# Optimization experiments

Measured on AMD Instinct MI355X. Metric: run time of the kernel, lower is better.

Reference implementation:

```python
import jax, jax.numpy as jnp
import numpy as np

IN_CHANNELS = 1024
NUM_HEADS = 16
HEAD_DIM = IN_CHANNELS // NUM_HEADS  # 64
N = 65536


def setup_inputs() -> dict:
    key = jax.random.key(0)
    k_x, k_wq, k_bq, k_wo, k_bo = jax.random.split(key, 5)
    x = jax.random.normal(k_x, (N, IN_CHANNELS), dtype=jnp.float32)
    # torch Linear convention: weight is [out_features, in_features]
    w_qkv = jax.random.normal(k_wq, (3 * IN_CHANNELS, IN_CHANNELS), dtype=jnp.float32) * 0.02
    b_qkv = jax.random.normal(k_bq, (3 * IN_CHANNELS,), dtype=jnp.float32) * 0.02
    w_out = jax.random.normal(k_wo, (IN_CHANNELS, IN_CHANNELS), dtype=jnp.float32) * 0.02
    b_out = jax.random.normal(k_bo, (IN_CHANNELS,), dtype=jnp.float32) * 0.02
    return {"x": x, "w_qkv": w_qkv, "b_qkv": b_qkv, "w_out": w_out, "b_out": b_out}


def reference(x, w_qkv, b_qkv, w_out, b_out):
    n = x.shape[0]
    scale = HEAD_DIM ** (-0.5)
    qkv = x @ w_qkv.T + b_qkv                       # [N, 3C]
    qkv = qkv.reshape(n, NUM_HEADS, 3 * HEAD_DIM)    # [N, H, 3D]
    q, k, v = jnp.split(qkv, 3, axis=-1)             # each [N, H, D]
    # attention over the HEAD dimension: [N, H, H] tiny score matrices
    attn = jnp.einsum('nhd,ngd->nhg', q * scale, k)
    attn = jax.nn.softmax(attn, axis=-1)
    out = jnp.einsum('nhg,ngd->nhd', attn, v)        # [N, H, D]
    out = out.reshape(n, NUM_HEADS * HEAD_DIM)       # [N, C]
    return out @ w_out.T + b_out
```

## Files before the change

### kernel.cpp

```cpp
#include <hip/hip_runtime.h>
#include <hip/hip_bf16.h>

#define N_TOK 65536
#define C_DIM 1024

typedef __hip_bfloat16 bf16;
typedef short short8 __attribute__((ext_vector_type(8)));
typedef short short4v __attribute__((ext_vector_type(4)));
typedef float f32x4 __attribute__((ext_vector_type(4)));

__device__ __forceinline__ void gload_lds16(const void* g, void* l) {
  __builtin_amdgcn_global_load_lds(
      (const __attribute__((address_space(1))) void*)g,
      (__attribute__((address_space(3))) void*)l, 16, 0, 0);
}

__global__ void cvt_kernel(const float* __restrict__ in, bf16* __restrict__ out, long n4) {
  long i = (long)blockIdx.x * blockDim.x + threadIdx.x;
  const long stride = (long)gridDim.x * blockDim.x;
  for (; i < n4; i += stride) {
    const float4 v = ((const float4*)in)[i];
    union { bf16 h[4]; uint2 u; } p;
    p.h[0] = __float2bfloat16(v.x);
    p.h[1] = __float2bfloat16(v.y);
    p.h[2] = __float2bfloat16(v.z);
    p.h[3] = __float2bfloat16(v.w);
    ((uint2*)out)[i] = p.u;
  }
}

template<bool OUT_BF16>
__global__ __launch_bounds__(256, 2) void gemm_bt(
    const bf16* __restrict__ A, const bf16* __restrict__ B,
    const float* __restrict__ bias, void* __restrict__ Cv,
    int M, int N, int K, int ntiles) {
  __shared__ __attribute__((aligned(16))) bf16 As[2][128 * 32];
  __shared__ __attribute__((aligned(16))) bf16 Bs[2][128 * 32];
  const int t = threadIdx.x;
  const int bid = blockIdx.x;
  const int mt = bid / ntiles, ntl = bid % ntiles;
  const long m0 = (long)mt * 128, n0 = (long)ntl * 128;
  const bf16* Ab = A + m0 * K;
  const bf16* Bb = B + n0 * K;

  const int lane = t & 63, wid = t >> 6;
  const int wr = (wid >> 1) * 64, wc = (wid & 1) * 64;
  const int lr = lane & 15, lk = (lane >> 4) * 8;

  f32x4 acc[4][4];
#pragma unroll
  for (int i = 0; i < 4; i++)
#pragma unroll
    for (int j = 0; j < 4; j++) acc[i][j] = f32x4{0.f, 0.f, 0.f, 0.f};

  auto stage = [&](int buf, int kt) {
    const long kbase = (long)kt * 32;
#pragma unroll
    for (int r = 0; r < 2; ++r) {
      const int lin = r * 256 + t;
      const int mrow = lin >> 2, ke = (lin & 3) * 8;
      gload_lds16(Ab + (long)mrow * K + kbase + ke, &As[buf][lin * 8]);
      gload_lds16(Bb + (long)mrow * K + kbase + ke, &Bs[buf][lin * 8]);
    }
  };

  stage(0, 0);
  const int KT = K / 32;
  int cur = 0;
  for (int kt = 0; kt < KT; ++kt) {
    __syncthreads();
    if (kt + 1 < KT) stage(cur ^ 1, kt + 1);
    short8 a[4], b[4];
#pragma unroll
    for (int i = 0; i < 4; i++)
      a[i] = *(const short8*)&As[cur][(wr + i * 16 + lr) * 32 + lk];
#pragma unroll
    for (int j = 0; j < 4; j++)
      b[j] = *(const short8*)&Bs[cur][(wc + j * 16 + lr) * 32 + lk];
#pragma unroll
    for (int i = 0; i < 4; i++)
#pragma unroll
      for (int j = 0; j < 4; j++)
        acc[i][j] = __builtin_amdgcn_mfma_f32_16x16x32_bf16(a[i], b[j], acc[i][j], 0, 0, 0);
    cur ^= 1;
  }

  float bv[4];
#pragma unroll
  for (int j = 0; j < 4; j++) bv[j] = bias[n0 + wc + j * 16 + lr];
#pragma unroll
  for (int i = 0; i < 4; i++) {
    const long rbase = m0 + wr + i * 16 + ((lane >> 4) << 2);
#pragma unroll
    for (int q = 0; q < 4; q++) {
      const long row = rbase + q;
#pragma unroll
      for (int j = 0; j < 4; j++) {
        const float v = acc[i][j][q] + bv[j];
        const long col = n0 + wc + j * 16 + lr;
        if constexpr (OUT_BF16)
          ((bf16*)Cv)[row * N + col] = __float2bfloat16(v);
        else
          ((float*)Cv)[row * N + col] = v;
      }
    }
  }
}

__global__ __launch_bounds__(256) void attn_kernel(const bf16* __restrict__ qkv,
                                                   bf16* __restrict__ out) {
  const int t = threadIdx.x, w = t >> 6, lane = t & 63;
  const long tok = (long)blockIdx.x * 4 + w;
  const bf16* base = qkv + tok * 3072;
  const int r = lane & 15, g4 = lane >> 4;

  const short8 ka0 = *(const short8*)(base + r * 192 + 64 + g4 * 8);
  const short8 ka1 = *(const short8*)(base + r * 192 + 96 + g4 * 8);
  const short8 qb0 = *(const short8*)(base + r * 192 + g4 * 8);
  const short8 qb1 = *(const short8*)(base + r * 192 + 32 + g4 * 8);
  f32x4 c = {0.f, 0.f, 0.f, 0.f};
  c = __builtin_amdgcn_mfma_f32_16x16x32_bf16(ka0, qb0, c, 0, 0, 0);
  c = __builtin_amdgcn_mfma_f32_16x16x32_bf16(ka1, qb1, c, 0, 0, 0);

  float s0 = c[0] * 0.125f, s1 = c[1] * 0.125f, s2 = c[2] * 0.125f, s3 = c[3] * 0.125f;
  float mx = fmaxf(fmaxf(s0, s1), fmaxf(s2, s3));
  mx = fmaxf(mx, __shfl_xor(mx, 16, 64));
  mx = fmaxf(mx, __shfl_xor(mx, 32, 64));
  const float e0 = __expf(s0 - mx), e1 = __expf(s1 - mx);
  const float e2 = __expf(s2 - mx), e3 = __expf(s3 - mx);
  float sum = e0 + e1 + e2 + e3;
  sum += __shfl_xor(sum, 16, 64);
  sum += __shfl_xor(sum, 32, 64);
  const float inv = 1.0f / sum;

#if __has_builtin(__builtin_amdgcn_mfma_f32_16x16x16bf16_1k)
  union { bf16 h[4]; short4v v; } pa;
  pa.h[0] = __float2bfloat16(e0 * inv);
  pa.h[1] = __float2bfloat16(e1 * inv);
  pa.h[2] = __float2bfloat16(e2 * inv);
  pa.h[3] = __float2bfloat16(e3 * inv);
#pragma unroll
  for (int ch = 0; ch < 4; ++ch) {
    union { bf16 h[4]; short4v v; } vb;
#pragma unroll
    for (int j = 0; j < 4; j++)
      vb.h[j] = base[(g4 * 4 + j) * 192 + 128 + ch * 16 + r];
    f32x4 o = {0.f, 0.f, 0.f, 0.f};
    o = __builtin_amdgcn_mfma_f32_16x16x16bf16_1k(pa.v, vb.v, o, 0, 0, 0);
#pragma unroll
    for (int i = 0; i < 4; i++)
      out[tok * 1024 + (g4 * 4 + i) * 64 + ch * 16 + r] = __float2bfloat16(o[i]);
  }
#else
  __shared__ float sm[4][16][16];
#pragma unroll
  for (int i = 0; i < 4; i++) sm[w][g4 * 4 + i][r] = ((i == 0) ? e0 : (i == 1) ? e1 : (i == 2) ? e2 : e3) * inv;
  __syncthreads();
  const int d = lane;
  float o[16];
#pragma unroll
  for (int h = 0; h < 16; h++) o[h] = 0.f;
  for (int g = 0; g < 16; g++) {
    const float vg = __bfloat162float(base[g * 192 + 128 + d]);
#pragma unroll
    for (int h = 0; h < 16; h++) o[h] += sm[w][g][h] * vg;
  }
#pragma unroll
  for (int h = 0; h < 16; h++) out[tok * 1024 + h * 64 + d] = __float2bfloat16(o[h]);
#endif
}

extern "C" void kernel_launch(void* const* d_in, const int* in_sizes, int n_in,
                              void* d_out, int out_size, void* d_ws, size_t ws_size,
                              hipStream_t stream) {
  const float* x     = (const float*)d_in[0];
  const float* w_qkv = (const float*)d_in[1];
  const float* b_qkv = (const float*)d_in[2];
  const float* w_out = (const float*)d_in[3];
  const float* b_out = (const float*)d_in[4];
  float* outp = (float*)d_out;

  char* ws = (char*)d_ws;
  bf16* x_b   = (bf16*)(ws);
  bf16* wq_b  = (bf16*)(ws + 134217728L);
  bf16* wo_b  = (bf16*)(ws + 140509184L);
  bf16* qkv_b = (bf16*)(ws + 142606336L);
  bf16* att_b = (bf16*)(ws + 545259520L);

  cvt_kernel<<<2048, 256, 0, stream>>>(x, x_b, (long)N_TOK * C_DIM / 4);
  cvt_kernel<<<768, 256, 0, stream>>>(w_qkv, wq_b, (long)3 * C_DIM * C_DIM / 4);
  cvt_kernel<<<256, 256, 0, stream>>>(w_out, wo_b, (long)C_DIM * C_DIM / 4);

  gemm_bt<true><<<512 * 24, 256, 0, stream>>>(x_b, wq_b, b_qkv, qkv_b,
                                              N_TOK, 3 * C_DIM, C_DIM, 24);
  attn_kernel<<<N_TOK / 4, 256, 0, stream>>>(qkv_b, att_b);
  gemm_bt<false><<<512 * 8, 256, 0, stream>>>(att_b, wo_b, b_out, outp,
                                              N_TOK, C_DIM, C_DIM, 8);
}
```

Before: 1.251 ms.

## Replace 128x128 GEMM with 256x256 tile, 8-wave, swizzled LDS pipelined kernel

Both GEMMs now use a 256x256 output tile computed by 512 threads (8 waves), with a K-step of 64 and double-buffered LDS. The LDS layout is XOR-swizzled to avoid bank conflicts, and an explicit vmcnt/barrier schedule staggers the A/B prefetch across four compute phases. s_setprio is raised around the MFMA bursts, and block IDs are remapped for L2 locality. The goal is more data reuse per byte loaded and better overlap of loads with MFMA. The cost is much higher register and LDS use (128 KB LDS per block) and fragile hand-written wait counts.

New measurement: 1.148 ms. 1.09x faster.

```diff
diff --git a/kernel.cpp b/kernel.cpp
--- a/kernel.cpp
+++ b/kernel.cpp
@@ -9,11 +9,19 @@
 typedef short short4v __attribute__((ext_vector_type(4)));
 typedef float f32x4 __attribute__((ext_vector_type(4)));
 
-__device__ __forceinline__ void gload_lds16(const void* g, void* l) {
+__device__ __forceinline__ void gload_lds16(const bf16* g, bf16* l) {
   __builtin_amdgcn_global_load_lds(
       (const __attribute__((address_space(1))) void*)g,
       (__attribute__((address_space(3))) void*)l, 16, 0, 0);
 }
+
+__device__ __forceinline__ void barrier_raw() {
+  asm volatile("" ::: "memory");
+  __builtin_amdgcn_s_barrier();
+  asm volatile("" ::: "memory");
+}
+
+#define VMCNT(n) asm volatile("s_waitcnt vmcnt(" #n ")" ::: "memory")
 
 __global__ void cvt_kernel(const float* __restrict__ in, bf16* __restrict__ out, long n4) {
   long i = (long)blockIdx.x * blockDim.x + threadIdx.x;
@@ -30,74 +38,152 @@
 }
 
 template<bool OUT_BF16>
-__global__ __launch_bounds__(256, 2) void gemm_bt(
+__global__ __launch_bounds__(512, 2) void gemm256(
     const bf16* __restrict__ A, const bf16* __restrict__ B,
     const float* __restrict__ bias, void* __restrict__ Cv,
-    int M, int N, int K, int ntiles) {
-  __shared__ __attribute__((aligned(16))) bf16 As[2][128 * 32];
-  __shared__ __attribute__((aligned(16))) bf16 Bs[2][128 * 32];
+    int M, int N, int K, int ntm) {
+  __shared__ __attribute__((aligned(16))) bf16 As[2][2][128 * 64];
+  __shared__ __attribute__((aligned(16))) bf16 Bs[2][2][128 * 64];
+
   const int t = threadIdx.x;
+  const int lane = t & 63, wid = t >> 6;
+  const int wr = wid >> 2, wc = wid & 3;
+  const int lr = lane & 15, g = lane >> 4;
+
+  const int nwg = gridDim.x;
   const int bid = blockIdx.x;
-  const int mt = bid / ntiles, ntl = bid % ntiles;
-  const long m0 = (long)mt * 128, n0 = (long)ntl * 128;
-  const bf16* Ab = A + m0 * K;
-  const bf16* Bb = B + n0 * K;
-
-  const int lane = t & 63, wid = t >> 6;
-  const int wr = (wid >> 1) * 64, wc = (wid & 1) * 64;
-  const int lr = lane & 15, lk = (lane >> 4) * 8;
-
-  f32x4 acc[4][4];
-#pragma unroll
-  for (int i = 0; i < 4; i++)
-#pragma unroll
-    for (int j = 0; j < 4; j++) acc[i][j] = f32x4{0.f, 0.f, 0.f, 0.f};
-
-  auto stage = [&](int buf, int kt) {
-    const long kbase = (long)kt * 32;
-#pragma unroll
-    for (int r = 0; r < 2; ++r) {
-      const int lin = r * 256 + t;
-      const int mrow = lin >> 2, ke = (lin & 3) * 8;
-      gload_lds16(Ab + (long)mrow * K + kbase + ke, &As[buf][lin * 8]);
-      gload_lds16(Bb + (long)mrow * K + kbase + ke, &Bs[buf][lin * 8]);
-    }
+  const int swz = (bid & 7) * (nwg >> 3) + (bid >> 3);
+  const int mt = swz % ntm;
+  const int nt = swz / ntm;
+  const long m0 = (long)mt * 256, n0 = (long)nt * 256;
+
+  const bf16* Abase = A + m0 * K;
+  const bf16* Bbase = B + n0 * K;
+
+  const int srow = t >> 3;
+  const int scol = (((t & 7) << 4) ^ ((srow & 7) << 4)) >> 1;
+  const int ldst = t * 8;
+
+  const int axor = (lr & 7) << 4;
+  const int colk0 = ((0 + g * 16) ^ axor) >> 1;
+  const int colk1 = ((64 + g * 16) ^ axor) >> 1;
+  const int brow0 = (wc & 1) * 64;
+
+  auto stageA = [&](int tt, int h) {
+    bf16* dst = &As[tt & 1][h][0];
+    const bf16* src = Abase + (long)(h * 128 + srow) * K + (long)tt * 64 + scol;
+    gload_lds16(src, dst + ldst);
+    gload_lds16(src + 64L * K, dst + 4096 + ldst);
   };
-
-  stage(0, 0);
-  const int KT = K / 32;
-  int cur = 0;
-  for (int kt = 0; kt < KT; ++kt) {
-    __syncthreads();
-    if (kt + 1 < KT) stage(cur ^ 1, kt + 1);
-    short8 a[4], b[4];
-#pragma unroll
-    for (int i = 0; i < 4; i++)
-      a[i] = *(const short8*)&As[cur][(wr + i * 16 + lr) * 32 + lk];
-#pragma unroll
-    for (int j = 0; j < 4; j++)
-      b[j] = *(const short8*)&Bs[cur][(wc + j * 16 + lr) * 32 + lk];
-#pragma unroll
-    for (int i = 0; i < 4; i++)
-#pragma unroll
-      for (int j = 0; j < 4; j++)
-        acc[i][j] = __builtin_amdgcn_mfma_f32_16x16x32_bf16(a[i], b[j], acc[i][j], 0, 0, 0);
-    cur ^= 1;
-  }
-
+  auto stageB = [&](int tt, int h) {
+    bf16* dst = &Bs[tt & 1][h][0];
+    const bf16* src = Bbase + (long)(h * 128 + srow) * K + (long)tt * 64 + scol;
+    gload_lds16(src, dst + 4096 * 0 + ldst);
+    gload_lds16(src + 64L * K, dst + 4096 + ldst);
+  };
+
+  f32x4 acc[8][4];
+#pragma unroll
+  for (int m = 0; m < 8; ++m)
+#pragma unroll
+    for (int n = 0; n < 4; ++n) acc[m][n] = f32x4{0.f, 0.f, 0.f, 0.f};
+
+  const int KT = K >> 6;
+  stageB(0, 0); stageB(0, 1);
+  stageA(0, 0); stageA(0, 1);
+  stageB(1, 0); stageB(1, 1);
+
+  short8 af[4][2], bq[4][2];
+
+  for (int tt = 0; tt < KT; ++tt) {
+    const int d = tt & 1;
+    const bf16* Ah = &As[d][wr][0];
+    const bf16* Bh = &Bs[d][wc >> 1][0];
+
+    if (tt < KT - 1) { VMCNT(4); } else { VMCNT(0); }
+    barrier_raw();
+#pragma unroll
+    for (int m = 0; m < 4; ++m) {
+      af[m][0] = *(const short8*)&Ah[(m * 16 + lr) * 64 + colk0];
+      af[m][1] = *(const short8*)&Ah[(m * 16 + lr) * 64 + colk1];
+    }
+#pragma unroll
+    for (int n = 0; n < 2; ++n) {
+      bq[n][0] = *(const short8*)&Bh[(brow0 + n * 16 + lr) * 64 + colk0];
+      bq[n][1] = *(const short8*)&Bh[(brow0 + n * 16 + lr) * 64 + colk1];
+    }
+    if (tt + 1 < KT) stageA(tt + 1, 0);
+    __builtin_amdgcn_s_setprio(1);
+#pragma unroll
+    for (int m = 0; m < 4; ++m)
+#pragma unroll
+      for (int n = 0; n < 2; ++n) {
+        acc[m][n] = __builtin_amdgcn_mfma_f32_16x16x32_bf16(af[m][0], bq[n][0], acc[m][n], 0, 0, 0);
+        acc[m][n] = __builtin_amdgcn_mfma_f32_16x16x32_bf16(af[m][1], bq[n][1], acc[m][n], 0, 0, 0);
+      }
+    __builtin_amdgcn_s_setprio(0);
+
+    barrier_raw();
+#pragma unroll
+    for (int n = 2; n < 4; ++n) {
+      bq[n][0] = *(const short8*)&Bh[(brow0 + n * 16 + lr) * 64 + colk0];
+      bq[n][1] = *(const short8*)&Bh[(brow0 + n * 16 + lr) * 64 + colk1];
+    }
+    if (tt + 1 < KT) stageA(tt + 1, 1);
+    __builtin_amdgcn_s_setprio(1);
+#pragma unroll
+    for (int m = 0; m < 4; ++m)
+#pragma unroll
+      for (int n = 2; n < 4; ++n) {
+        acc[m][n] = __builtin_amdgcn_mfma_f32_16x16x32_bf16(af[m][0], bq[n][0], acc[m][n], 0, 0, 0);
+        acc[m][n] = __builtin_amdgcn_mfma_f32_16x16x32_bf16(af[m][1], bq[n][1], acc[m][n], 0, 0, 0);
+      }
+    __builtin_amdgcn_s_setprio(0);
+
+    barrier_raw();
+#pragma unroll
+    for (int m = 0; m < 4; ++m) {
+      af[m][0] = *(const short8*)&Ah[((m + 4) * 16 + lr) * 64 + colk0];
+      af[m][1] = *(const short8*)&Ah[((m + 4) * 16 + lr) * 64 + colk1];
+    }
+    if (tt + 2 < KT) stageB(tt + 2, 0);
+    __builtin_amdgcn_s_setprio(1);
+#pragma unroll
+    for (int m = 0; m < 4; ++m)
+#pragma unroll
+      for (int n = 0; n < 2; ++n) {
+        acc[m + 4][n] = __builtin_amdgcn_mfma_f32_16x16x32_bf16(af[m][0], bq[n][0], acc[m + 4][n], 0, 0, 0);
+        acc[m + 4][n] = __builtin_amdgcn_mfma_f32_16x16x32_bf16(af[m][1], bq[n][1], acc[m + 4][n], 0, 0, 0);
+      }
+    __builtin_amdgcn_s_setprio(0);
+
+    barrier_raw();
+    if (tt + 2 < KT) stageB(tt + 2, 1);
+    __builtin_amdgcn_s_setprio(1);
+#pragma unroll
+    for (int m = 0; m < 4; ++m)
+#pragma unroll
+      for (int n = 2; n < 4; ++n) {
+        acc[m + 4][n] = __builtin_amdgcn_mfma_f32_16x16x32_bf16(af[m][0], bq[n][0], acc[m + 4][n], 0, 0, 0);
+        acc[m + 4][n] = __builtin_amdgcn_mfma_f32_16x16x32_bf16(af[m][1], bq[n][1], acc[m + 4][n], 0, 0, 0);
+      }
+    __builtin_amdgcn_s_setprio(0);
+  }
+
+  const long orow0 = m0 + wr * 128;
+  const long ocol0 = n0 + wc * 64;
   float bv[4];
 #pragma unroll
-  for (int j = 0; j < 4; j++) bv[j] = bias[n0 + wc + j * 16 + lr];
-#pragma unroll
-  for (int i = 0; i < 4; i++) {
-    const long rbase = m0 + wr + i * 16 + ((lane >> 4) << 2);
-#pragma unroll
-    for (int q = 0; q < 4; q++) {
-      const long row = rbase + q;
-#pragma unroll
-      for (int j = 0; j < 4; j++) {
-        const float v = acc[i][j][q] + bv[j];
-        const long col = n0 + wc + j * 16 + lr;
+  for (int n = 0; n < 4; ++n) bv[n] = bias[ocol0 + n * 16 + lr];
+#pragma unroll
+  for (int m = 0; m < 8; ++m) {
+#pragma unroll
+    for (int q = 0; q < 4; ++q) {
+      const long row = orow0 + m * 16 + g * 4 + q;
+#pragma unroll
+      for (int n = 0; n < 4; ++n) {
+        const float v = acc[m][n][q] + bv[n];
+        const long col = ocol0 + n * 16 + lr;
         if constexpr (OUT_BF16)
           ((bf16*)Cv)[row * N + col] = __float2bfloat16(v);
         else
@@ -133,7 +219,6 @@
   sum += __shfl_xor(sum, 32, 64);
   const float inv = 1.0f / sum;
 
-#if __has_builtin(__builtin_amdgcn_mfma_f32_16x16x16bf16_1k)
   union { bf16 h[4]; short4v v; } pa;
   pa.h[0] = __float2bfloat16(e0 * inv);
   pa.h[1] = __float2bfloat16(e1 * inv);
@@ -151,23 +236,6 @@
     for (int i = 0; i < 4; i++)
       out[tok * 1024 + (g4 * 4 + i) * 64 + ch * 16 + r] = __float2bfloat16(o[i]);
   }
-#else
-  __shared__ float sm[4][16][16];
-#pragma unroll
-  for (int i = 0; i < 4; i++) sm[w][g4 * 4 + i][r] = ((i == 0) ? e0 : (i == 1) ? e1 : (i == 2) ? e2 : e3) * inv;
-  __syncthreads();
-  const int d = lane;
-  float o[16];
-#pragma unroll
-  for (int h = 0; h < 16; h++) o[h] = 0.f;
-  for (int g = 0; g < 16; g++) {
-    const float vg = __bfloat162float(base[g * 192 + 128 + d]);
-#pragma unroll
-    for (int h = 0; h < 16; h++) o[h] += sm[w][g][h] * vg;
-  }
-#pragma unroll
-  for (int h = 0; h < 16; h++) out[tok * 1024 + h * 64 + d] = __float2bfloat16(o[h]);
-#endif
 }
 
 extern "C" void kernel_launch(void* const* d_in, const int* in_sizes, int n_in,
@@ -191,9 +259,9 @@
   cvt_kernel<<<768, 256, 0, stream>>>(w_qkv, wq_b, (long)3 * C_DIM * C_DIM / 4);
   cvt_kernel<<<256, 256, 0, stream>>>(w_out, wo_b, (long)C_DIM * C_DIM / 4);
 
-  gemm_bt<true><<<512 * 24, 256, 0, stream>>>(x_b, wq_b, b_qkv, qkv_b,
-                                              N_TOK, 3 * C_DIM, C_DIM, 24);
+  gemm256<true><<<(N_TOK / 256) * (3 * C_DIM / 256), 512, 0, stream>>>(
+      x_b, wq_b, b_qkv, qkv_b, N_TOK, 3 * C_DIM, C_DIM, N_TOK / 256);
   attn_kernel<<<N_TOK / 4, 256, 0, stream>>>(qkv_b, att_b);
-  gemm_bt<false><<<512 * 8, 256, 0, stream>>>(att_b, wo_b, b_out, outp,
-                                              N_TOK, C_DIM, C_DIM, 8);
-}
+  gemm256<false><<<(N_TOK / 256) * (C_DIM / 256), 512, 0, stream>>>(
+      att_b, wo_b, b_out, outp, N_TOK, C_DIM, C_DIM, N_TOK / 256);
+}
```
